# Kernel tuning notes

Hardware: AMD Instinct MI355X
Metric: run time of the kernel (lower is better)

The kernel has to match this reference:

```python
import jax, jax.numpy as jnp
import numpy as np

B, T, N = 32, 2048, 2048
D, L, TE, H = 512, 256, 1024, 8

def _ln(x, g, b, eps=1e-5):
    m = x.mean(-1, keepdims=True)
    v = ((x - m) ** 2).mean(-1, keepdims=True)
    return (x - m) / jnp.sqrt(v + eps) * g + b

def setup_inputs() -> dict:
    key = jax.random.key(0)
    ks = jax.random.split(key, 12)
    s = 0.02
    return {
        "x": jax.random.normal(ks[0], (B, T, D), jnp.float32),
        "xf": jax.random.normal(ks[1], (B, N, L), jnp.float32),
        "emb": jax.random.normal(ks[2], (B, TE), jnp.float32),
        "norm_g": jnp.ones((D,), jnp.float32),
        "norm_b": jnp.zeros((D,), jnp.float32),
        "tnorm_g": jnp.ones((L,), jnp.float32),
        "tnorm_b": jnp.zeros((L,), jnp.float32),
        "Wq": jax.random.normal(ks[3], (D, D), jnp.float32) * s,
        "bq": jnp.zeros((D,), jnp.float32),
        "Wk": jax.random.normal(ks[4], (L, D), jnp.float32) * s,
        "bk": jnp.zeros((D,), jnp.float32),
        "Wv": jax.random.normal(ks[5], (L, D), jnp.float32) * s,
        "bv": jnp.zeros((D,), jnp.float32),
        "We": jax.random.normal(ks[6], (TE, 2 * D), jnp.float32) * s,
        "be": jnp.zeros((2 * D,), jnp.float32),
        "snorm_g": jnp.ones((D,), jnp.float32),
        "snorm_b": jnp.zeros((D,), jnp.float32),
        "Wo": jax.random.normal(ks[7], (D, D), jnp.float32) * s,
        "bo": jnp.zeros((D,), jnp.float32),
    }

def reference(x, xf, emb, norm_g, norm_b, tnorm_g, tnorm_b, Wq, bq, Wk, bk, Wv, bv,
              We, be, snorm_g, snorm_b, Wo, bo):
    b, t, d = x.shape
    n = xf.shape[1]
    hd = d // H
    # projections with pre-LayerNorms
    q = (_ln(x, norm_g, norm_b) @ Wq + bq).reshape(b, t, H, hd)
    xfn = _ln(xf, tnorm_g, tnorm_b)
    k = (xfn @ Wk + bk).reshape(b, n, H, hd)
    v = (xfn @ Wv + bv).reshape(b, n, H, hd)
    # dual softmax of linear attention: query over head-dim, key over sequence
    q = jax.nn.softmax(q, axis=-1)
    k = jax.nn.softmax(k, axis=1)
    # O(N*d^2) linear attention
    attn = jnp.einsum('bnhd,bnhl->bhdl', k, v)          # [B,H,hd,hd]
    y = jnp.einsum('bthd,bhdl->bthl', q, attn).reshape(b, t, d)
    # StylizationBlock (dropout is identity in eval)
    emb_out = jax.nn.silu(emb) @ We + be                # [B, 2D]
    scale, shift = emb_out[:, None, :d], emb_out[:, None, d:]
    h = _ln(y, snorm_g, snorm_b) * (1.0 + scale) + shift
    h = jax.nn.silu(h) @ Wo + bo
    return x + h
```

## Files before the change

kernel.cpp:

```cpp
#include <hip/hip_runtime.h>
#include <math.h>

#define B_ 32
#define T_ 2048
#define N_ 2048
#define D_ 512
#define L_ 256
#define TE_ 1024
#define H_ 8
#define MROWS 65536
#define KCH 16
#define NC_ 8

typedef __attribute__((ext_vector_type(8))) short short8;
typedef __attribute__((ext_vector_type(4))) float f32x4;

__device__ __forceinline__ unsigned short f2bf(float f) {
  unsigned u = __float_as_uint(f);
  unsigned r = (u + 0x7FFF + ((u >> 16) & 1)) >> 16;
  return (unsigned short)r;
}
__device__ __forceinline__ float bf2f(unsigned short u) {
  return __uint_as_float(((unsigned)u) << 16);
}
__device__ __forceinline__ void gload_lds16(const void* g, void* l) {
  __builtin_amdgcn_global_load_lds(
      (const __attribute__((address_space(1))) void*)g,
      (__attribute__((address_space(3))) void*)l, 16, 0, 0);
}

__device__ __forceinline__ float blockReduceSum(float v, float* ws) {
#pragma unroll
  for (int m = 32; m >= 1; m >>= 1) v += __shfl_xor(v, m, 64);
  int wid = threadIdx.x >> 6;
  int lane = threadIdx.x & 63;
  __syncthreads();
  if (lane == 0) ws[wid] = v;
  __syncthreads();
  return ws[0] + ws[1] + ws[2] + ws[3];
}

template <int COLS>
__global__ void __launch_bounds__(256) ln_rows(const float* __restrict__ in,
                                               const float* __restrict__ g,
                                               const float* __restrict__ bb,
                                               unsigned short* __restrict__ out) {
  constexpr int E = COLS / 256;
  __shared__ float ws[4];
  size_t row = blockIdx.x;
  const float* rp = in + row * COLS;
  float v[E];
  float s = 0.f;
#pragma unroll
  for (int e = 0; e < E; ++e) {
    v[e] = rp[threadIdx.x + e * 256];
    s += v[e];
  }
  s = blockReduceSum(s, ws);
  float mean = s * (1.0f / COLS);
  float q = 0.f;
#pragma unroll
  for (int e = 0; e < E; ++e) {
    float d = v[e] - mean;
    q += d * d;
  }
  q = blockReduceSum(q, ws);
  float rstd = rsqrtf(q * (1.0f / COLS) + 1e-5f);
  unsigned short* op = out + row * COLS;
#pragma unroll
  for (int e = 0; e < E; ++e) {
    int c = threadIdx.x + e * 256;
    op[c] = f2bf((v[e] - mean) * rstd * g[c] + bb[c]);
  }
}

__global__ void __launch_bounds__(256) transcast(const float* __restrict__ W,
                                                 unsigned short* __restrict__ Wt,
                                                 int K, int Ncols) {
  __shared__ float t[32][33];
  int k0 = blockIdx.x * 32, n0 = blockIdx.y * 32;
  int tx = threadIdx.x & 31, ty = threadIdx.x >> 5;
#pragma unroll
  for (int i = 0; i < 32; i += 8)
    t[ty + i][tx] = W[(size_t)(k0 + ty + i) * Ncols + n0 + tx];
  __syncthreads();
#pragma unroll
  for (int i = 0; i < 32; i += 8)
    Wt[(size_t)(n0 + ty + i) * K + k0 + tx] = f2bf(t[tx][ty + i]);
}

template <int KT, bool ADD, bool OUTBF, bool QSM>
__global__ void __launch_bounds__(256) gemm_mfma(const unsigned short* __restrict__ A,
                                                 const unsigned short* __restrict__ Wt,
                                                 const float* __restrict__ bias,
                                                 const float* __restrict__ add,
                                                 void* __restrict__ Cv) {
  __shared__ __align__(16) unsigned short sA[2][128 * 32];
  __shared__ __align__(16) unsigned short sB[2][128 * 32];
  int tid = threadIdx.x;
  int w = tid >> 6, lane = tid & 63;
  int quad = lane >> 4, r16 = lane & 15;
  int wr = w >> 1, wc = w & 1;
  size_t m0 = (size_t)blockIdx.y * 128;
  int n0 = blockIdx.x * 128;
  int srow = lane >> 2;
  int scol = (lane & 3) * 8;
  f32x4 acc[4][4] = {};

  const unsigned short* Arow0 = &A[(m0 + w * 32 + srow) * KT + scol];
  const unsigned short* Brow0 = &Wt[(size_t)(n0 + w * 32 + srow) * KT + scol];

#define G_STAGE(buf, k0)                                                          \
  do {                                                                            \
    gload_lds16(Arow0 + (k0), &sA[buf][(w * 2 + 0) * 512]);                       \
    gload_lds16(Arow0 + (size_t)16 * KT + (k0), &sA[buf][(w * 2 + 1) * 512]);     \
    gload_lds16(Brow0 + (k0), &sB[buf][(w * 2 + 0) * 512]);                       \
    gload_lds16(Brow0 + (size_t)16 * KT + (k0), &sB[buf][(w * 2 + 1) * 512]);     \
  } while (0)

#define G_COMPUTE(buf)                                                            \
  do {                                                                            \
    short8 af[4], bfr[4];                                                         \
    _Pragma("unroll") for (int mi = 0; mi < 4; ++mi)                              \
        af[mi] = *(const short8*)&sA[buf][(wr * 64 + mi * 16 + r16) * 32 + quad * 8]; \
    _Pragma("unroll") for (int ni = 0; ni < 4; ++ni)                              \
        bfr[ni] = *(const short8*)&sB[buf][(wc * 64 + ni * 16 + r16) * 32 + quad * 8]; \
    _Pragma("unroll") for (int mi = 0; mi < 4; ++mi)                              \
        _Pragma("unroll") for (int ni = 0; ni < 4; ++ni)                          \
            acc[mi][ni] =                                                         \
                __builtin_amdgcn_mfma_f32_16x16x32_bf16(af[mi], bfr[ni], acc[mi][ni], 0, 0, 0); \
  } while (0)

  constexpr int NT = KT / 32;
  G_STAGE(0, 0);
  __syncthreads();
#pragma unroll 1
  for (int t = 0; t < NT; t += 2) {
    if (t + 1 < NT) G_STAGE(1, (t + 1) * 32);
    G_COMPUTE(0);
    __syncthreads();
    if (t + 2 < NT) G_STAGE(0, (t + 2) * 32);
    G_COMPUTE(1);
    __syncthreads();
  }
#undef G_STAGE
#undef G_COMPUTE

  float* Cf = (float*)Cv;
  unsigned short* Cb = (unsigned short*)Cv;
#pragma unroll
  for (int mi = 0; mi < 4; ++mi)
#pragma unroll
    for (int r = 0; r < 4; ++r) {
      size_t grow = m0 + wr * 64 + mi * 16 + quad * 4 + r;
      if constexpr (QSM) {
        float v4[4];
        float mx = -1e30f;
#pragma unroll
        for (int ni = 0; ni < 4; ++ni) {
          v4[ni] = acc[mi][ni][r] + bias[n0 + wc * 64 + ni * 16 + r16];
          mx = fmaxf(mx, v4[ni]);
        }
#pragma unroll
        for (int s = 8; s >= 1; s >>= 1) mx = fmaxf(mx, __shfl_xor(mx, s, 64));
        float ssum = 0.f;
#pragma unroll
        for (int ni = 0; ni < 4; ++ni) {
          v4[ni] = expf(v4[ni] - mx);
          ssum += v4[ni];
        }
#pragma unroll
        for (int s = 8; s >= 1; s >>= 1) ssum += __shfl_xor(ssum, s, 64);
        float inv = 1.f / ssum;
#pragma unroll
        for (int ni = 0; ni < 4; ++ni) {
          int gcol = n0 + wc * 64 + ni * 16 + r16;
          Cb[grow * 512 + gcol] = f2bf(v4[ni] * inv);
        }
      } else {
#pragma unroll
        for (int ni = 0; ni < 4; ++ni) {
          int gcol = n0 + wc * 64 + ni * 16 + r16;
          float val = acc[mi][ni][r] + bias[gcol];
          if constexpr (ADD) val += add[grow * 512 + gcol];
          if constexpr (OUTBF)
            Cb[grow * 512 + gcol] = f2bf(val);
          else
            Cf[grow * 512 + gcol] = val;
        }
      }
    }
}

__global__ void __launch_bounds__(256) kstats_part(const float* __restrict__ k,
                                                   float* __restrict__ pmax,
                                                   float* __restrict__ psum) {
  int b = blockIdx.x, cg = blockIdx.y, ch = blockIdx.z;
  int tid = threadIdx.x;
  int lane = tid & 63, slice = tid >> 6;
  int c = cg * 64 + lane;
  constexpr int ROWS = N_ / KCH;
  constexpr int PT = ROWS / 4;
  const float* kp = k + ((size_t)b * N_ + (size_t)ch * ROWS) * D_ + c;
  float v[PT];
#pragma unroll
  for (int i = 0; i < PT; ++i) v[i] = kp[(size_t)(slice + i * 4) * D_];
  float m = v[0];
#pragma unroll
  for (int i = 1; i < PT; ++i) m = fmaxf(m, v[i]);
  float s = 0.f;
#pragma unroll
  for (int i = 0; i < PT; ++i) s += expf(v[i] - m);
  __shared__ float mred[256], sred[256];
  mred[tid] = m;
  sred[tid] = s;
  __syncthreads();
  if (tid < 64) {
    float m0 = mred[tid], m1 = mred[tid + 64], m2 = mred[tid + 128], m3 = mred[tid + 192];
    float mm = fmaxf(fmaxf(m0, m1), fmaxf(m2, m3));
    float ss = sred[tid] * expf(m0 - mm) + sred[tid + 64] * expf(m1 - mm) +
               sred[tid + 128] * expf(m2 - mm) + sred[tid + 192] * expf(m3 - mm);
    pmax[((size_t)b * KCH + ch) * D_ + cg * 64 + tid] = mm;
    psum[((size_t)b * KCH + ch) * D_ + cg * 64 + tid] = ss;
  }
}

__global__ void __launch_bounds__(256) kstats_comb(const float* __restrict__ pmax,
                                                   const float* __restrict__ psum,
                                                   float* __restrict__ kmax,
                                                   float* __restrict__ ksum) {
  int b = blockIdx.x;
  int c = blockIdx.y * 256 + threadIdx.x;
  float pm[KCH];
#pragma unroll
  for (int ch = 0; ch < KCH; ++ch) pm[ch] = pmax[((size_t)b * KCH + ch) * D_ + c];
  float m = pm[0];
#pragma unroll
  for (int ch = 1; ch < KCH; ++ch) m = fmaxf(m, pm[ch]);
  float s = 0.f;
#pragma unroll
  for (int ch = 0; ch < KCH; ++ch)
    s += psum[((size_t)b * KCH + ch) * D_ + c] * expf(pm[ch] - m);
  kmax[b * D_ + c] = m;
  ksum[b * D_ + c] = s;
}

__global__ void __launch_bounds__(256) attn_part_kernel(const float* __restrict__ k,
                                                        const float* __restrict__ v,
                                                        const float* __restrict__ kmax,
                                                        const float* __restrict__ ksum,
                                                        float* __restrict__ part) {
  int b = blockIdx.x, h = blockIdx.y, nc = blockIdx.z;
  int tid = threadIdx.x;
  __shared__ float ks_[32][68];
  __shared__ float vs_[32][68];
  __shared__ float mx[64], is_[64];
  if (tid < 64) {
    mx[tid] = kmax[b * D_ + h * 64 + tid];
    is_[tid] = 1.f / ksum[b * D_ + h * 64 + tid];
  }
  const float* kp = k + ((size_t)b * N_ + nc * 256) * D_ + h * 64;
  const float* vp = v + ((size_t)b * N_ + nc * 256) * D_ + h * 64;
  float acc[4][4] = {};
  int tx = tid & 15, ty = tid >> 4;
  int lr = tid >> 4;
  int c4 = (tid & 15) * 4;
  float4 kv0, vv0, kv1, vv1;
  kv0 = *(const float4*)&kp[(size_t)lr * D_ + c4];
  vv0 = *(const float4*)&vp[(size_t)lr * D_ + c4];
  kv1 = *(const float4*)&kp[(size_t)(lr + 16) * D_ + c4];
  vv1 = *(const float4*)&vp[(size_t)(lr + 16) * D_ + c4];
  for (int n0 = 0; n0 < 256; n0 += 32) {
    __syncthreads();
    ks_[lr][c4 + 0] = expf(kv0.x - mx[c4 + 0]) * is_[c4 + 0];
    ks_[lr][c4 + 1] = expf(kv0.y - mx[c4 + 1]) * is_[c4 + 1];
    ks_[lr][c4 + 2] = expf(kv0.z - mx[c4 + 2]) * is_[c4 + 2];
    ks_[lr][c4 + 3] = expf(kv0.w - mx[c4 + 3]) * is_[c4 + 3];
    vs_[lr][c4 + 0] = vv0.x;
    vs_[lr][c4 + 1] = vv0.y;
    vs_[lr][c4 + 2] = vv0.z;
    vs_[lr][c4 + 3] = vv0.w;
    ks_[lr + 16][c4 + 0] = expf(kv1.x - mx[c4 + 0]) * is_[c4 + 0];
    ks_[lr + 16][c4 + 1] = expf(kv1.y - mx[c4 + 1]) * is_[c4 + 1];
    ks_[lr + 16][c4 + 2] = expf(kv1.z - mx[c4 + 2]) * is_[c4 + 2];
    ks_[lr + 16][c4 + 3] = expf(kv1.w - mx[c4 + 3]) * is_[c4 + 3];
    vs_[lr + 16][c4 + 0] = vv1.x;
    vs_[lr + 16][c4 + 1] = vv1.y;
    vs_[lr + 16][c4 + 2] = vv1.z;
    vs_[lr + 16][c4 + 3] = vv1.w;
    if (n0 + 32 < 256) {
      kv0 = *(const float4*)&kp[(size_t)(n0 + 32 + lr) * D_ + c4];
      vv0 = *(const float4*)&vp[(size_t)(n0 + 32 + lr) * D_ + c4];
      kv1 = *(const float4*)&kp[(size_t)(n0 + 48 + lr) * D_ + c4];
      vv1 = *(const float4*)&vp[(size_t)(n0 + 48 + lr) * D_ + c4];
    }
    __syncthreads();
#pragma unroll
    for (int nn = 0; nn < 32; ++nn) {
      float av[4], bv2[4];
#pragma unroll
      for (int i = 0; i < 4; ++i) av[i] = ks_[nn][ty * 4 + i];
#pragma unroll
      for (int j = 0; j < 4; ++j) bv2[j] = vs_[nn][tx * 4 + j];
#pragma unroll
      for (int i = 0; i < 4; ++i)
#pragma unroll
        for (int j = 0; j < 4; ++j) acc[i][j] += av[i] * bv2[j];
    }
  }
  float* ap = part + ((size_t)(b * H_ + h) * NC_ + nc) * 4096;
#pragma unroll
  for (int i = 0; i < 4; ++i) {
    float4 st = make_float4(acc[i][0], acc[i][1], acc[i][2], acc[i][3]);
    *(float4*)&ap[(ty * 4 + i) * 64 + tx * 4] = st;
  }
}

__global__ void __launch_bounds__(256) attn_reduce(const float* __restrict__ part,
                                                   unsigned short* __restrict__ attnT) {
  size_t o = ((size_t)blockIdx.x * 256 + threadIdx.x) * 4;
  size_t bh = o >> 12;
  size_t e = o & 4095;
  float4 s = make_float4(0.f, 0.f, 0.f, 0.f);
#pragma unroll
  for (int nc = 0; nc < NC_; ++nc) {
    float4 p = *(const float4*)&part[(bh * NC_ + nc) * 4096 + e];
    s.x += p.x;
    s.y += p.y;
    s.z += p.z;
    s.w += p.w;
  }
  int d = (int)(e >> 6);
  int l = (int)(e & 63);
  unsigned short* ab = attnT + bh * 4096;
  ab[(l + 0) * 64 + d] = f2bf(s.x);
  ab[(l + 1) * 64 + d] = f2bf(s.y);
  ab[(l + 2) * 64 + d] = f2bf(s.z);
  ab[(l + 3) * 64 + d] = f2bf(s.w);
}

__global__ void __launch_bounds__(256) embmod(const float* __restrict__ emb,
                                              const float* __restrict__ We,
                                              const float* __restrict__ be,
                                              float* __restrict__ eo) {
  int b = blockIdx.x, tid = threadIdx.x;
  __shared__ float se[TE_];
  for (int i = tid; i < TE_; i += 256) {
    float e = emb[b * TE_ + i];
    se[i] = e / (1.f + expf(-e));
  }
  __syncthreads();
  int j0 = tid * 4;
  float a0 = 0, a1 = 0, a2 = 0, a3 = 0;
  for (int i = 0; i < TE_; ++i) {
    float s = se[i];
    float4 wv = *(const float4*)&We[(size_t)i * 1024 + j0];
    a0 += s * wv.x;
    a1 += s * wv.y;
    a2 += s * wv.z;
    a3 += s * wv.w;
  }
  eo[b * 1024 + j0 + 0] = a0 + be[j0 + 0];
  eo[b * 1024 + j0 + 1] = a1 + be[j0 + 1];
  eo[b * 1024 + j0 + 2] = a2 + be[j0 + 2];
  eo[b * 1024 + j0 + 3] = a3 + be[j0 + 3];
}

__global__ void __launch_bounds__(256) yein_mfma(const unsigned short* __restrict__ qsm,
                                                 const unsigned short* __restrict__ attnT,
                                                 float* __restrict__ y) {
  int b = blockIdx.z, h = blockIdx.y;
  size_t t0 = (size_t)blockIdx.x * 256;
  int tid = threadIdx.x;
  int w = tid >> 6, lane = tid & 63;
  int quad = lane >> 4, r16 = lane & 15;
  int srow = lane >> 2;
  int scol = (lane & 3) * 8;
  __shared__ __align__(16) unsigned short sA[2][256 * 32];
  __shared__ __align__(16) unsigned short sB[2][64 * 32];
  const unsigned short* qp = qsm + ((size_t)b * T_ + t0) * D_ + h * 64;
  const unsigned short* bp = attnT + (size_t)(b * H_ + h) * 4096;
  f32x4 acc[4][4] = {};

#pragma unroll
  for (int half = 0; half < 2; ++half) {
    int k0 = half * 32;
#pragma unroll
    for (int i = 0; i < 4; ++i) {
      int seg = w * 4 + i;
      gload_lds16(&qp[(size_t)(seg * 16 + srow) * D_ + k0 + scol], &sA[half][seg * 512]);
    }
    gload_lds16(&bp[(w * 16 + srow) * 64 + k0 + scol], &sB[half][w * 512]);
  }
  __syncthreads();
#pragma unroll
  for (int half = 0; half < 2; ++half) {
    short8 af[4], bfr[4];
#pragma unroll
    for (int mi = 0; mi < 4; ++mi)
      af[mi] = *(const short8*)&sA[half][(w * 64 + mi * 16 + r16) * 32 + quad * 8];
#pragma unroll
    for (int ni = 0; ni < 4; ++ni)
      bfr[ni] = *(const short8*)&sB[half][(ni * 16 + r16) * 32 + quad * 8];
#pragma unroll
    for (int mi = 0; mi < 4; ++mi)
#pragma unroll
      for (int ni = 0; ni < 4; ++ni)
        acc[mi][ni] = __builtin_amdgcn_mfma_f32_16x16x32_bf16(af[mi], bfr[ni], acc[mi][ni], 0, 0, 0);
  }

#pragma unroll
  for (int mi = 0; mi < 4; ++mi)
#pragma unroll
    for (int r = 0; r < 4; ++r) {
      size_t grow = t0 + w * 64 + mi * 16 + quad * 4 + r;
      float* yp = y + ((size_t)b * T_ + grow) * D_ + h * 64;
#pragma unroll
      for (int ni = 0; ni < 4; ++ni) yp[ni * 16 + r16] = acc[mi][ni][r];
    }
}

__global__ void __launch_bounds__(256) modln(const float* __restrict__ y,
                                             const float* __restrict__ sg,
                                             const float* __restrict__ sb,
                                             const float* __restrict__ eo,
                                             unsigned short* __restrict__ hs) {
  __shared__ float ws[4];
  size_t row = blockIdx.x;
  int b = (int)(row >> 11);
  const float* rp = y + row * D_;
  float v[2];
  float s = 0.f;
#pragma unroll
  for (int e = 0; e < 2; ++e) {
    v[e] = rp[threadIdx.x + e * 256];
    s += v[e];
  }
  s = blockReduceSum(s, ws);
  float mean = s * (1.0f / D_);
  float q = 0.f;
#pragma unroll
  for (int e = 0; e < 2; ++e) {
    float d = v[e] - mean;
    q += d * d;
  }
  q = blockReduceSum(q, ws);
  float rstd = rsqrtf(q * (1.0f / D_) + 1e-5f);
#pragma unroll
  for (int e = 0; e < 2; ++e) {
    int c = threadIdx.x + e * 256;
    float xm = (v[e] - mean) * rstd * sg[c] + sb[c];
    float sc = eo[b * 1024 + c];
    float sh = eo[b * 1024 + D_ + c];
    float hm = xm * (1.f + sc) + sh;
    hs[row * D_ + c] = f2bf(hm / (1.f + expf(-hm)));
  }
}

extern "C" void kernel_launch(void* const* d_in, const int* in_sizes, int n_in,
                              void* d_out, int out_size, void* d_ws, size_t ws_size,
                              hipStream_t stream) {
  const float* x = (const float*)d_in[0];
  const float* xf = (const float*)d_in[1];
  const float* emb = (const float*)d_in[2];
  const float* norm_g = (const float*)d_in[3];
  const float* norm_b = (const float*)d_in[4];
  const float* tnorm_g = (const float*)d_in[5];
  const float* tnorm_b = (const float*)d_in[6];
  const float* Wq = (const float*)d_in[7];
  const float* bq = (const float*)d_in[8];
  const float* Wk = (const float*)d_in[9];
  const float* bk = (const float*)d_in[10];
  const float* Wv = (const float*)d_in[11];
  const float* bv = (const float*)d_in[12];
  const float* We = (const float*)d_in[13];
  const float* be = (const float*)d_in[14];
  const float* sg = (const float*)d_in[15];
  const float* sb = (const float*)d_in[16];
  const float* Wo = (const float*)d_in[17];
  const float* bo = (const float*)d_in[18];
  float* out = (float*)d_out;

  float* w = (float*)d_ws;
  unsigned short* qbf = (unsigned short*)w;
  float* kbuf = w + 16777216;
  float* vbuf = w + 16777216 + 33554432;
  unsigned short* xnbf = (unsigned short*)(w + 83886080);
  unsigned short* xfnbf = (unsigned short*)(w + 100663296);
  unsigned short* attnT = (unsigned short*)(w + 109051904);
  float* kmaxp = w + 109051904 + 1048576;
  float* ksump = kmaxp + 16384;
  float* embout = ksump + 16384;
  unsigned short* wqt = (unsigned short*)(embout + 32768);
  unsigned short* wkt = wqt + 262144;
  unsigned short* wvt = wkt + 131072;
  unsigned short* wot = wvt + 131072;
  float* pmaxp = w + 83886080;
  float* psump = pmaxp + (size_t)B_ * KCH * D_;
  float* attnpart = w + 100663296;

  transcast<<<dim3(16, 16), 256, 0, stream>>>(Wq, wqt, 512, 512);
  transcast<<<dim3(8, 16), 256, 0, stream>>>(Wk, wkt, 256, 512);
  transcast<<<dim3(8, 16), 256, 0, stream>>>(Wv, wvt, 256, 512);
  transcast<<<dim3(16, 16), 256, 0, stream>>>(Wo, wot, 512, 512);
  ln_rows<512><<<MROWS, 256, 0, stream>>>(x, norm_g, norm_b, xnbf);
  gemm_mfma<512, false, true, true><<<dim3(4, 512), 256, 0, stream>>>(xnbf, wqt, bq, nullptr, qbf);
  ln_rows<256><<<MROWS, 256, 0, stream>>>(xf, tnorm_g, tnorm_b, xfnbf);
  gemm_mfma<256, false, false, false><<<dim3(4, 512), 256, 0, stream>>>(xfnbf, wkt, bk, nullptr, kbuf);
  gemm_mfma<256, false, false, false><<<dim3(4, 512), 256, 0, stream>>>(xfnbf, wvt, bv, nullptr, vbuf);
  kstats_part<<<dim3(32, 8, KCH), 256, 0, stream>>>(kbuf, pmaxp, psump);
  kstats_comb<<<dim3(32, 2), 256, 0, stream>>>(pmaxp, psump, kmaxp, ksump);
  attn_part_kernel<<<dim3(32, 8, NC_), 256, 0, stream>>>(kbuf, vbuf, kmaxp, ksump, attnpart);
  attn_reduce<<<1024, 256, 0, stream>>>(attnpart, attnT);
  embmod<<<32, 256, 0, stream>>>(emb, We, be, embout);
  yein_mfma<<<dim3(8, 8, 32), 256, 0, stream>>>(qbf, attnT, kbuf);
  modln<<<MROWS, 256, 0, stream>>>(kbuf, sg, sb, embout, xnbf);
  gemm_mfma<512, true, false, false><<<dim3(4, 512), 256, 0, stream>>>(xnbf, wot, bo, x, out);
}
```

Before: 926.3 us.

## Store K/V in bf16 and fuse key softmax stats into K GEMM epilogue

The K and V projection GEMMs now write bf16 instead of fp32, which halves their write traffic and the read traffic in attn_part. The K GEMM epilogue computes per-128-row partial column max and sum-exp, and attn_part combines the 16 partials itself, so the kstats_part and kstats_comb kernels and the extra fp32 K read are gone. The four weight transpose-casts are merged into one launch. In exchange, precision is lower for K and V, and the K epilogue does extra exp work plus a block sync.

```diff
diff --git a/kernel.cpp b/kernel.cpp
--- a/kernel.cpp
+++ b/kernel.cpp
@@ -14,6 +14,7 @@
 
 typedef __attribute__((ext_vector_type(8))) short short8;
 typedef __attribute__((ext_vector_type(4))) float f32x4;
+typedef __attribute__((ext_vector_type(4))) unsigned short us4;
 
 __device__ __forceinline__ unsigned short f2bf(float f) {
   unsigned u = __float_as_uint(f);
@@ -74,27 +75,43 @@
   }
 }
 
-__global__ void __launch_bounds__(256) transcast(const float* __restrict__ W,
-                                                 unsigned short* __restrict__ Wt,
-                                                 int K, int Ncols) {
+__global__ void __launch_bounds__(256) transcast_all(const float* __restrict__ Wq,
+                                                     const float* __restrict__ Wk,
+                                                     const float* __restrict__ Wv,
+                                                     const float* __restrict__ Wo,
+                                                     unsigned short* __restrict__ wqt,
+                                                     unsigned short* __restrict__ wkt,
+                                                     unsigned short* __restrict__ wvt,
+                                                     unsigned short* __restrict__ wot) {
+  int z = blockIdx.z;
+  const float* W;
+  unsigned short* Wt;
+  int K;
+  if (z == 0) { W = Wq; Wt = wqt; K = 512; }
+  else if (z == 1) { W = Wk; Wt = wkt; K = 256; }
+  else if (z == 2) { W = Wv; Wt = wvt; K = 256; }
+  else { W = Wo; Wt = wot; K = 512; }
+  int k0 = blockIdx.x * 32, n0 = blockIdx.y * 32;
+  if (k0 >= K) return;
   __shared__ float t[32][33];
-  int k0 = blockIdx.x * 32, n0 = blockIdx.y * 32;
   int tx = threadIdx.x & 31, ty = threadIdx.x >> 5;
 #pragma unroll
   for (int i = 0; i < 32; i += 8)
-    t[ty + i][tx] = W[(size_t)(k0 + ty + i) * Ncols + n0 + tx];
+    t[ty + i][tx] = W[(size_t)(k0 + ty + i) * 512 + n0 + tx];
   __syncthreads();
 #pragma unroll
   for (int i = 0; i < 32; i += 8)
     Wt[(size_t)(n0 + ty + i) * K + k0 + tx] = f2bf(t[tx][ty + i]);
 }
 
-template <int KT, bool ADD, bool OUTBF, bool QSM>
+template <int KT, bool ADD, bool OUTBF, bool QSM, bool KSTATS>
 __global__ void __launch_bounds__(256) gemm_mfma(const unsigned short* __restrict__ A,
                                                  const unsigned short* __restrict__ Wt,
                                                  const float* __restrict__ bias,
                                                  const float* __restrict__ add,
-                                                 void* __restrict__ Cv) {
+                                                 void* __restrict__ Cv,
+                                                 float* __restrict__ pmaxO,
+                                                 float* __restrict__ psumO) {
   __shared__ __align__(16) unsigned short sA[2][128 * 32];
   __shared__ __align__(16) unsigned short sB[2][128 * 32];
   int tid = threadIdx.x;
@@ -148,12 +165,13 @@
 
   float* Cf = (float*)Cv;
   unsigned short* Cb = (unsigned short*)Cv;
-#pragma unroll
-  for (int mi = 0; mi < 4; ++mi)
-#pragma unroll
-    for (int r = 0; r < 4; ++r) {
-      size_t grow = m0 + wr * 64 + mi * 16 + quad * 4 + r;
-      if constexpr (QSM) {
+
+  if constexpr (QSM) {
+#pragma unroll
+    for (int mi = 0; mi < 4; ++mi)
+#pragma unroll
+      for (int r = 0; r < 4; ++r) {
+        size_t grow = m0 + wr * 64 + mi * 16 + quad * 4 + r;
         float v4[4];
         float mx = -1e30f;
 #pragma unroll
@@ -177,7 +195,74 @@
           int gcol = n0 + wc * 64 + ni * 16 + r16;
           Cb[grow * 512 + gcol] = f2bf(v4[ni] * inv);
         }
-      } else {
+      }
+  } else if constexpr (KSTATS) {
+    float tmax[4], tsum[4];
+#pragma unroll
+    for (int ni = 0; ni < 4; ++ni) { tmax[ni] = -1e30f; tsum[ni] = 0.f; }
+#pragma unroll
+    for (int mi = 0; mi < 4; ++mi)
+#pragma unroll
+      for (int r = 0; r < 4; ++r) {
+        size_t grow = m0 + wr * 64 + mi * 16 + quad * 4 + r;
+#pragma unroll
+        for (int ni = 0; ni < 4; ++ni) {
+          int gcol = n0 + wc * 64 + ni * 16 + r16;
+          unsigned short bv = f2bf(acc[mi][ni][r] + bias[gcol]);
+          Cb[grow * 512 + gcol] = bv;
+          tmax[ni] = fmaxf(tmax[ni], bf2f(bv));
+        }
+      }
+#pragma unroll
+    for (int mi = 0; mi < 4; ++mi)
+#pragma unroll
+      for (int r = 0; r < 4; ++r)
+#pragma unroll
+        for (int ni = 0; ni < 4; ++ni) {
+          int gcol = n0 + wc * 64 + ni * 16 + r16;
+          float vr = bf2f(f2bf(acc[mi][ni][r] + bias[gcol]));
+          tsum[ni] += expf(vr - tmax[ni]);
+        }
+#pragma unroll
+    for (int ni = 0; ni < 4; ++ni) {
+#pragma unroll
+      for (int mask = 16; mask <= 32; mask <<= 1) {
+        float om = __shfl_xor(tmax[ni], mask, 64);
+        float os = __shfl_xor(tsum[ni], mask, 64);
+        float nm = fmaxf(tmax[ni], om);
+        tsum[ni] = tsum[ni] * expf(tmax[ni] - nm) + os * expf(om - nm);
+        tmax[ni] = nm;
+      }
+    }
+    __shared__ float smax[4][64], ssum2[4][64];
+    if (quad == 0) {
+#pragma unroll
+      for (int ni = 0; ni < 4; ++ni) {
+        smax[w][ni * 16 + r16] = tmax[ni];
+        ssum2[w][ni * 16 + r16] = tsum[ni];
+      }
+    }
+    __syncthreads();
+    if (w < 2 && quad == 0) {
+      int b = (int)(blockIdx.y >> 4), ch = (int)(blockIdx.y & 15);
+#pragma unroll
+      for (int ni = 0; ni < 4; ++ni) {
+        int i = ni * 16 + r16;
+        float m1 = smax[w][i], m2 = smax[w + 2][i];
+        float s1 = ssum2[w][i], s2 = ssum2[w + 2][i];
+        float nm = fmaxf(m1, m2);
+        float ss = s1 * expf(m1 - nm) + s2 * expf(m2 - nm);
+        size_t off = ((size_t)(b * KCH + ch)) * D_ + n0 + w * 64 + i;
+        pmaxO[off] = nm;
+        psumO[off] = ss;
+      }
+    }
+  } else {
+#pragma unroll
+    for (int mi = 0; mi < 4; ++mi)
+#pragma unroll
+      for (int r = 0; r < 4; ++r) {
+        size_t grow = m0 + wr * 64 + mi * 16 + quad * 4 + r;
 #pragma unroll
         for (int ni = 0; ni < 4; ++ni) {
           int gcol = n0 + wc * 64 + ni * 16 + r16;
@@ -189,110 +274,57 @@
             Cf[grow * 512 + gcol] = val;
         }
       }
-    }
-}
-
-__global__ void __launch_bounds__(256) kstats_part(const float* __restrict__ k,
-                                                   float* __restrict__ pmax,
-                                                   float* __restrict__ psum) {
-  int b = blockIdx.x, cg = blockIdx.y, ch = blockIdx.z;
-  int tid = threadIdx.x;
-  int lane = tid & 63, slice = tid >> 6;
-  int c = cg * 64 + lane;
-  constexpr int ROWS = N_ / KCH;
-  constexpr int PT = ROWS / 4;
-  const float* kp = k + ((size_t)b * N_ + (size_t)ch * ROWS) * D_ + c;
-  float v[PT];
-#pragma unroll
-  for (int i = 0; i < PT; ++i) v[i] = kp[(size_t)(slice + i * 4) * D_];
-  float m = v[0];
-#pragma unroll
-  for (int i = 1; i < PT; ++i) m = fmaxf(m, v[i]);
-  float s = 0.f;
-#pragma unroll
-  for (int i = 0; i < PT; ++i) s += expf(v[i] - m);
-  __shared__ float mred[256], sred[256];
-  mred[tid] = m;
-  sred[tid] = s;
-  __syncthreads();
-  if (tid < 64) {
-    float m0 = mred[tid], m1 = mred[tid + 64], m2 = mred[tid + 128], m3 = mred[tid + 192];
-    float mm = fmaxf(fmaxf(m0, m1), fmaxf(m2, m3));
-    float ss = sred[tid] * expf(m0 - mm) + sred[tid + 64] * expf(m1 - mm) +
-               sred[tid + 128] * expf(m2 - mm) + sred[tid + 192] * expf(m3 - mm);
-    pmax[((size_t)b * KCH + ch) * D_ + cg * 64 + tid] = mm;
-    psum[((size_t)b * KCH + ch) * D_ + cg * 64 + tid] = ss;
-  }
-}
-
-__global__ void __launch_bounds__(256) kstats_comb(const float* __restrict__ pmax,
-                                                   const float* __restrict__ psum,
-                                                   float* __restrict__ kmax,
-                                                   float* __restrict__ ksum) {
-  int b = blockIdx.x;
-  int c = blockIdx.y * 256 + threadIdx.x;
-  float pm[KCH];
-#pragma unroll
-  for (int ch = 0; ch < KCH; ++ch) pm[ch] = pmax[((size_t)b * KCH + ch) * D_ + c];
-  float m = pm[0];
-#pragma unroll
-  for (int ch = 1; ch < KCH; ++ch) m = fmaxf(m, pm[ch]);
-  float s = 0.f;
-#pragma unroll
-  for (int ch = 0; ch < KCH; ++ch)
-    s += psum[((size_t)b * KCH + ch) * D_ + c] * expf(pm[ch] - m);
-  kmax[b * D_ + c] = m;
-  ksum[b * D_ + c] = s;
-}
-
-__global__ void __launch_bounds__(256) attn_part_kernel(const float* __restrict__ k,
-                                                        const float* __restrict__ v,
-                                                        const float* __restrict__ kmax,
-                                                        const float* __restrict__ ksum,
+  }
+}
+
+__global__ void __launch_bounds__(256) attn_part_kernel(const unsigned short* __restrict__ k,
+                                                        const unsigned short* __restrict__ v,
+                                                        const float* __restrict__ pmax,
+                                                        const float* __restrict__ psum,
                                                         float* __restrict__ part) {
   int b = blockIdx.x, h = blockIdx.y, nc = blockIdx.z;
   int tid = threadIdx.x;
   __shared__ float ks_[32][68];
   __shared__ float vs_[32][68];
   __shared__ float mx[64], is_[64];
+  int lr = tid >> 4;
+  int c4 = (tid & 15) * 4;
+  const unsigned short* kp = k + ((size_t)b * N_ + nc * 256) * D_ + h * 64;
+  const unsigned short* vp = v + ((size_t)b * N_ + nc * 256) * D_ + h * 64;
+  us4 kv0 = *(const us4*)&kp[(size_t)lr * D_ + c4];
+  us4 vv0 = *(const us4*)&vp[(size_t)lr * D_ + c4];
+  us4 kv1 = *(const us4*)&kp[(size_t)(lr + 16) * D_ + c4];
+  us4 vv1 = *(const us4*)&vp[(size_t)(lr + 16) * D_ + c4];
   if (tid < 64) {
-    mx[tid] = kmax[b * D_ + h * 64 + tid];
-    is_[tid] = 1.f / ksum[b * D_ + h * 64 + tid];
-  }
-  const float* kp = k + ((size_t)b * N_ + nc * 256) * D_ + h * 64;
-  const float* vp = v + ((size_t)b * N_ + nc * 256) * D_ + h * 64;
+    int c = h * 64 + tid;
+    float m = -1e30f, s = 0.f;
+#pragma unroll
+    for (int ch = 0; ch < KCH; ++ch) {
+      float pm = pmax[((size_t)(b * KCH + ch)) * D_ + c];
+      float ps = psum[((size_t)(b * KCH + ch)) * D_ + c];
+      float nm = fmaxf(m, pm);
+      s = s * expf(m - nm) + ps * expf(pm - nm);
+      m = nm;
+    }
+    mx[tid] = m;
+    is_[tid] = 1.f / s;
+  }
   float acc[4][4] = {};
   int tx = tid & 15, ty = tid >> 4;
-  int lr = tid >> 4;
-  int c4 = (tid & 15) * 4;
-  float4 kv0, vv0, kv1, vv1;
-  kv0 = *(const float4*)&kp[(size_t)lr * D_ + c4];
-  vv0 = *(const float4*)&vp[(size_t)lr * D_ + c4];
-  kv1 = *(const float4*)&kp[(size_t)(lr + 16) * D_ + c4];
-  vv1 = *(const float4*)&vp[(size_t)(lr + 16) * D_ + c4];
   for (int n0 = 0; n0 < 256; n0 += 32) {
     __syncthreads();
-    ks_[lr][c4 + 0] = expf(kv0.x - mx[c4 + 0]) * is_[c4 + 0];
-    ks_[lr][c4 + 1] = expf(kv0.y - mx[c4 + 1]) * is_[c4 + 1];
-    ks_[lr][c4 + 2] = expf(kv0.z - mx[c4 + 2]) * is_[c4 + 2];
-    ks_[lr][c4 + 3] = expf(kv0.w - mx[c4 + 3]) * is_[c4 + 3];
-    vs_[lr][c4 + 0] = vv0.x;
-    vs_[lr][c4 + 1] = vv0.y;
-    vs_[lr][c4 + 2] = vv0.z;
-    vs_[lr][c4 + 3] = vv0.w;
-    ks_[lr + 16][c4 + 0] = expf(kv1.x - mx[c4 + 0]) * is_[c4 + 0];
-    ks_[lr + 16][c4 + 1] = expf(kv1.y - mx[c4 + 1]) * is_[c4 + 1];
-    ks_[lr + 16][c4 + 2] = expf(kv1.z - mx[c4 + 2]) * is_[c4 + 2];
-    ks_[lr + 16][c4 + 3] = expf(kv1.w - mx[c4 + 3]) * is_[c4 + 3];
-    vs_[lr + 16][c4 + 0] = vv1.x;
-    vs_[lr + 16][c4 + 1] = vv1.y;
-    vs_[lr + 16][c4 + 2] = vv1.z;
-    vs_[lr + 16][c4 + 3] = vv1.w;
+#pragma unroll
+    for (int j = 0; j < 4; ++j) {
+      ks_[lr][c4 + j] = expf(bf2f(kv0[j]) - mx[c4 + j]) * is_[c4 + j];
+      vs_[lr][c4 + j] = bf2f(vv0[j]);
+      ks_[lr + 16][c4 + j] = expf(bf2f(kv1[j]) - mx[c4 + j]) * is_[c4 + j];
+      vs_[lr + 16][c4 + j] = bf2f(vv1[j]);
+    }
     if (n0 + 32 < 256) {
-      kv0 = *(const float4*)&kp[(size_t)(n0 + 32 + lr) * D_ + c4];
-      vv0 = *(const float4*)&vp[(size_t)(n0 + 32 + lr) * D_ + c4];
-      kv1 = *(const float4*)&kp[(size_t)(n0 + 48 + lr) * D_ + c4];
-      vv1 = *(const float4*)&vp[(size_t)(n0 + 48 + lr) * D_ + c4];
+      kv0 = *(const us4*)&kp[(size_t)(n0 + 32 + lr) * D_ + c4];
+      vv0 = *(const us4*)&vp[(size_t)(n0 + 32 + lr) * D_ + c4];
+      kv1 = *(const us4*)&kp[(size_t)(n0 + 48 + lr) * D_ + c4];
+      vv1 = *(const us4*)&vp[(size_t)(n0 + 48 + lr) * D_ + c4];
     }
     __syncthreads();
 #pragma unroll
@@ -483,37 +515,35 @@
 
   float* w = (float*)d_ws;
   unsigned short* qbf = (unsigned short*)w;
-  float* kbuf = w + 16777216;
-  float* vbuf = w + 16777216 + 33554432;
+  unsigned short* kb = (unsigned short*)(w + 16777216);
+  unsigned short* vb = (unsigned short*)(w + 33554432);
+  float* ybuf = w + 50331648;
   unsigned short* xnbf = (unsigned short*)(w + 83886080);
   unsigned short* xfnbf = (unsigned short*)(w + 100663296);
+  float* attnpart = w + 100663296;
   unsigned short* attnT = (unsigned short*)(w + 109051904);
-  float* kmaxp = w + 109051904 + 1048576;
-  float* ksump = kmaxp + 16384;
-  float* embout = ksump + 16384;
+  float* pmaxp = w + 109051904 + 524288;
+  float* psump = pmaxp + 262144;
+  float* embout = psump + 262144;
   unsigned short* wqt = (unsigned short*)(embout + 32768);
   unsigned short* wkt = wqt + 262144;
   unsigned short* wvt = wkt + 131072;
   unsigned short* wot = wvt + 131072;
-  float* pmaxp = w + 83886080;
-  float* psump = pmaxp + (size_t)B_ * KCH * D_;
-  float* attnpart = w + 100663296;
-
-  transcast<<<dim3(16, 16), 256, 0, stream>>>(Wq, wqt, 512, 512);
-  transcast<<<dim3(8, 16), 256, 0, stream>>>(Wk, wkt, 256, 512);
-  transcast<<<dim3(8, 16), 256, 0, stream>>>(Wv, wvt, 256, 512);
-  transcast<<<dim3(16, 16), 256, 0, stream>>>(Wo, wot, 512, 512);
+
+  transcast_all<<<dim3(16, 16, 4), 256, 0, stream>>>(Wq, Wk, Wv, Wo, wqt, wkt, wvt, wot);
   ln_rows<512><<<MROWS, 256, 0, stream>>>(x, norm_g, norm_b, xnbf);
-  gemm_mfma<512, false, true, true><<<dim3(4, 512), 256, 0, stream>>>(xnbf, wqt, bq, nullptr, qbf);
+  gemm_mfma<512, false, true, true, false><<<dim3(4, 512), 256, 0, stream>>>(
+      xnbf, wqt, bq, nullptr, qbf, nullptr, nullptr);
   ln_rows<256><<<MROWS, 256, 0, stream>>>(xf, tnorm_g, tnorm_b, xfnbf);
-  gemm_mfma<256, false, false, false><<<dim3(4, 512), 256, 0, stream>>>(xfnbf, wkt, bk, nullptr, kbuf);
-  gemm_mfma<256, false, false, false><<<dim3(4, 512), 256, 0, stream>>>(xfnbf, wvt, bv, nullptr, vbuf);
-  kstats_part<<<dim3(32, 8, KCH), 256, 0, stream>>>(kbuf, pmaxp, psump);
-  kstats_comb<<<dim3(32, 2), 256, 0, stream>>>(pmaxp, psump, kmaxp, ksump);
-  attn_part_kernel<<<dim3(32, 8, NC_), 256, 0, stream>>>(kbuf, vbuf, kmaxp, ksump, attnpart);
+  gemm_mfma<256, false, true, false, true><<<dim3(4, 512), 256, 0, stream>>>(
+      xfnbf, wkt, bk, nullptr, kb, pmaxp, psump);
+  gemm_mfma<256, false, true, false, false><<<dim3(4, 512), 256, 0, stream>>>(
+      xfnbf, wvt, bv, nullptr, vb, nullptr, nullptr);
+  attn_part_kernel<<<dim3(32, 8, NC_), 256, 0, stream>>>(kb, vb, pmaxp, psump, attnpart);
   attn_reduce<<<1024, 256, 0, stream>>>(attnpart, attnT);
   embmod<<<32, 256, 0, stream>>>(emb, We, be, embout);
-  yein_mfma<<<dim3(8, 8, 32), 256, 0, stream>>>(qbf, attnT, kbuf);
-  modln<<<MROWS, 256, 0, stream>>>(kbuf, sg, sb, embout, xnbf);
-  gemm_mfma<512, true, false, false><<<dim3(4, 512), 256, 0, stream>>>(xnbf, wot, bo, x, out);
-}
+  yein_mfma<<<dim3(8, 8, 32), 256, 0, stream>>>(qbf, attnT, ybuf);
+  modln<<<MROWS, 256, 0, stream>>>(ybuf, sg, sb, embout, xnbf);
+  gemm_mfma<512, true, false, false, false><<<dim3(4, 512), 256, 0, stream>>>(
+      xnbf, wot, bo, x, out, nullptr, nullptr);
+}
```

Result: faster. 904.5 us (-2.3%).
